# Optimization experiments

Measured on AMD Instinct MI355X. Metric: run time of the kernel, lower is better.

## Reference

```python
import jax, jax.numpy as jnp
import numpy as np

L, BS, D, NH = 1024, 4, 1024, 16
DH = D // NH
H = max(DH, L)  # big=True in DenseSynthesizer -> h = max(head_dim, n_tokens)


def setup_inputs() -> dict:
    key = jax.random.key(0)
    ks = jax.random.split(key, 10)
    s = 0.02
    x = jax.random.normal(ks[0], (L, BS, D), dtype=jnp.float32)
    # additive causal mask (n_tokens, n_tokens)
    causal = jnp.tril(jnp.ones((L, L), dtype=bool))
    attention_mask = jnp.where(causal, 0.0, -1e9).astype(jnp.float32)
    Wi = jax.random.normal(ks[1], (2 * D, D), dtype=jnp.float32) * s
    bi = jnp.zeros((2 * D,), dtype=jnp.float32)
    w1 = jax.random.normal(ks[2], (NH, DH, H), dtype=jnp.float32) * s
    b1 = jnp.zeros((NH, H), dtype=jnp.float32)
    w2 = jax.random.normal(ks[3], (NH, H, L), dtype=jnp.float32) * s
    b2 = jnp.zeros((NH, L), dtype=jnp.float32)
    Wo = jax.random.normal(ks[4], (D, D), dtype=jnp.float32) * s
    bo = jnp.zeros((D,), dtype=jnp.float32)
    return {"x": x, "attention_mask": attention_mask, "Wi": Wi, "bi": bi,
            "w1": w1, "b1": b1, "w2": w2, "b2": b2, "Wo": Wo, "bo": bo}


def reference(x, attention_mask, Wi, bi, w1, b1, w2, b2, Wo, bo):
    l, bs, d = x.shape
    nh, dh, h = w1.shape
    # input projection, chunk into synthesizer input q and values v
    proj = x @ Wi.T + bi                                    # (l, bs, 2d)
    q, v = jnp.split(proj, 2, axis=-1)
    q = q.reshape(l, bs, nh, dh).transpose(1, 0, 2, 3)      # (bs, l, nh, dh)
    v = v.reshape(l, bs * nh, dh).transpose(1, 0, 2)        # (bs*nh, l, dh), n = b*nh + k
    # DenseSynthesizer: per-head two-layer MLP producing attention logits
    hid = jax.nn.relu(jnp.einsum('blkd,kdh->blkh', q, w1) + b1)
    logits = jnp.einsum('blkh,khm->blkm', hid, w2) + b2     # (bs, l, nh, n_tokens)
    logits = logits[..., :l]
    # faithful to torch transpose(0,3).view(l,l,bs*nh).transpose(0,2):
    # flattened batch-head index is m = k*bs + b (head-major)
    logits = logits.transpose(2, 0, 1, 3).reshape(bs * nh, l, l)
    logits = logits + attention_mask[None, :, :]
    probs = jax.nn.softmax(logits, axis=-1)                 # dropout p=0 (eval)
    out = jnp.matmul(probs, v)                              # (bs*nh, l, dh)
    out = out.transpose(1, 0, 2).reshape(l, bs, d)
    return out @ Wo.T + bo
```

## Files before the change

### kernel.cpp

```cpp
#include <hip/hip_runtime.h>

typedef unsigned short u16;
typedef short bf16x8 __attribute__((ext_vector_type(8)));
typedef float f32x4 __attribute__((ext_vector_type(4)));

#define BSZ 4
#define DD 1024
#define LLL 1024

__device__ __forceinline__ float bf2f(u16 u) {
    union { unsigned int i; float f; } w;
    w.i = ((unsigned int)u) << 16;
    return w.f;
}
__device__ __forceinline__ u16 f2bf(float f) {
    union { float fl; unsigned int i; } w;
    w.fl = f;
    w.i += 0x7fffu + ((w.i >> 16) & 1u);
    return (u16)(w.i >> 16);
}

__device__ __forceinline__ void load_lds16(const u16* g, u16* l) {
    __builtin_amdgcn_global_load_lds(
        (const __attribute__((address_space(1))) unsigned int*)g,
        (__attribute__((address_space(3))) unsigned int*)l, 16, 0, 0);
}

__global__ void cvt_all(const float* __restrict__ x, const float* __restrict__ Wi,
                        const float* __restrict__ Wo, u16* __restrict__ xb,
                        u16* __restrict__ wib, u16* __restrict__ wob) {
    int b = blockIdx.x;
    const float* in; u16* out;
    if (b < 4096)      { in = x;  out = xb; }
    else if (b < 6144) { in = Wi; out = wib; b -= 4096; }
    else               { in = Wo; out = wob; b -= 6144; }
    const size_t i = ((size_t)b * 256 + threadIdx.x) * 4;
    const float4 v = *(const float4*)(in + i);
    ushort4 o;
    o.x = f2bf(v.x); o.y = f2bf(v.y); o.z = f2bf(v.z); o.w = f2bf(v.w);
    *(ushort4*)(out + i) = o;
}

__global__ void transpose_cvt(const float* __restrict__ in, u16* __restrict__ out,
                              int R, int C) {
    __shared__ float tile[32][33];
    const size_t base = (size_t)blockIdx.z * R * C;
    const int c0 = blockIdx.x << 5, r0 = blockIdx.y << 5;
    const int tx = threadIdx.x & 31, ty = threadIdx.x >> 5;
    #pragma unroll
    for (int i = 0; i < 32; i += 8)
        tile[ty + i][tx] = in[base + (size_t)(r0 + ty + i) * C + c0 + tx];
    __syncthreads();
    #pragma unroll
    for (int i = 0; i < 32; i += 8)
        out[base + (size_t)(c0 + ty + i) * R + r0 + tx] = f2bf(tile[tx][ty + i]);
}

__global__ void build_vt(const u16* __restrict__ proj, u16* __restrict__ vt) {
    __shared__ u16 tile[64][66];
    const int t = threadIdx.x;
    const int m0 = blockIdx.x << 6;
    const int jj = blockIdx.y;
    const int b = jj >> 4, k = jj & 15;
    const int tx = t & 63, ty = t >> 6;
    #pragma unroll
    for (int mi = ty; mi < 64; mi += 4)
        tile[mi][tx] = proj[(size_t)((m0 + mi) * BSZ + b) * 2048 + 1024 + k * 64 + tx];
    __syncthreads();
    #pragma unroll
    for (int di = ty; di < 64; di += 4)
        vt[((size_t)jj * 80 + di) * 1024 + m0 + tx] = tile[tx][di];
    #pragma unroll
    for (int di = 64 + ty; di < 80; di += 4)
        vt[((size_t)jj * 80 + di) * 1024 + m0 + tx] = (di == 64) ? 0x3F80 : 0;
}

template<int OUT_F32, int RELU>
__global__ __launch_bounds__(256, 2) void gemm_bf16_nt(
    const u16* __restrict__ A, int lda, long long sA,
    const u16* __restrict__ B, int ldb, long long sB,
    const float* __restrict__ bias, int sBias,
    void* __restrict__ C, int ldc, long long sC,
    int K)
{
    __shared__ u16 As[128 * 64];
    __shared__ u16 Bs[128 * 64];
    const int t = threadIdx.x;
    const int z = blockIdx.z;
    const u16* Ab = A + (size_t)z * sA + (size_t)blockIdx.x * 128 * lda;
    const u16* Bb = B + (size_t)z * sB + (size_t)blockIdx.y * 128 * ldb;
    const int wave = t >> 6, lane = t & 63;
    const int wrow = (wave >> 1) << 6;
    const int wcol = (wave & 1) << 6;
    const int lr = lane & 15, lq = lane >> 4;
    const int srow = t >> 3;
    const int gchunk = (t & 7) ^ (srow & 7);
    const u16* ApG = Ab + (size_t)srow * lda + gchunk * 8;
    const u16* BpG = Bb + (size_t)srow * ldb + gchunk * 8;
    u16* AsD = &As[t * 8];
    u16* BsD = &Bs[t * 8];
    const int o0 = ((lq    ) ^ (lr & 7)) * 8;
    const int o1 = ((lq + 4) ^ (lr & 7)) * 8;

    f32x4 acc[4][4];
    #pragma unroll
    for (int i = 0; i < 4; i++)
        #pragma unroll
        for (int j = 0; j < 4; j++)
            acc[i][j] = (f32x4){0.f, 0.f, 0.f, 0.f};

    for (int k0 = 0; k0 < K; k0 += 64) {
        __syncthreads();
        #pragma unroll
        for (int j = 0; j < 4; j++) {
            load_lds16(ApG + (size_t)j * 32 * lda + k0, AsD + j * 2048);
            load_lds16(BpG + (size_t)j * 32 * ldb + k0, BsD + j * 2048);
        }
        __syncthreads();
        #pragma unroll
        for (int s = 0; s < 2; s++) {
            const int oo = s ? o1 : o0;
            bf16x8 af[4], bfv[4];
            #pragma unroll
            for (int i = 0; i < 4; i++)
                af[i] = *(const bf16x8*)&As[(wrow + i * 16 + lr) * 64 + oo];
            #pragma unroll
            for (int j = 0; j < 4; j++)
                bfv[j] = *(const bf16x8*)&Bs[(wcol + j * 16 + lr) * 64 + oo];
            #pragma unroll
            for (int i = 0; i < 4; i++)
                #pragma unroll
                for (int j = 0; j < 4; j++)
                    acc[i][j] = __builtin_amdgcn_mfma_f32_16x16x32_bf16(
                        af[i], bfv[j], acc[i][j], 0, 0, 0);
        }
    }

    const float* biasb = bias + (size_t)z * sBias;
    const size_t row0 = (size_t)blockIdx.x * 128 + wrow + lq * 4;
    const int col0 = blockIdx.y * 128 + wcol + lr;
    #pragma unroll
    for (int j = 0; j < 4; j++) {
        const int col = col0 + j * 16;
        const float bb = biasb[col];
        #pragma unroll
        for (int i = 0; i < 4; i++) {
            #pragma unroll
            for (int r = 0; r < 4; r++) {
                const size_t row = row0 + i * 16 + r;
                float v = acc[i][j][r] + bb;
                if (RELU) v = fmaxf(v, 0.f);
                const size_t idx = row * (size_t)ldc + col;
                if (OUT_F32) ((float*)C)[(size_t)z * sC + idx] = v;
                else         ((u16*)C)[(size_t)z * sC + idx] = f2bf(v);
            }
        }
    }
}

__global__ __launch_bounds__(256, 2) void fused_attn(
    const u16* __restrict__ hid,
    const u16* __restrict__ w2t,
    const float* __restrict__ b2,
    const u16* __restrict__ vt,
    u16* __restrict__ attn)
{
    __shared__ u16 As[64 * 64];
    __shared__ u16 Bs[256 * 64];
    __shared__ u16 Ps[64 * 264];
    const int t = threadIdx.x;
    const int kq = blockIdx.x;
    const int pair = blockIdx.y;
    const int wave = t >> 6, lane = t & 63;
    const int lr = lane & 15, lq = lane >> 4;
    const int wi = wave >> 1, wj = wave & 1;
    const int srow = t >> 3;
    const int gch = (t & 7) ^ (srow & 7);
    const int o0 = ((lq    ) ^ (lr & 7)) * 8;
    const int o1 = ((lq + 4) ^ (lr & 7)) * 8;
    const int bv = kq >> 2;
    const int kvb = 4 * (kq & 3);
    const u16* hb = hid + (size_t)kq * 4194304;
    const u16* wb = w2t + (size_t)kq * 1048576 + (size_t)srow * 1024 + gch * 8;
    const float* b2b = b2 + kq * 1024;

    for (int part = 0; part < 2; part++) {
        const int s = part ? (63 - pair) : pair;
        const int l0 = s << 4;
        const int nt = (s >> 4) + 1;
        const u16* ApG0 = hb + (size_t)((l0 + (srow & 15)) * 4 + (srow >> 4)) * 1024 + gch * 8;
        const u16* ApG1 = ApG0 + (size_t)2 * 1024;
        f32x4 o[5];
        #pragma unroll
        for (int j = 0; j < 5; j++) o[j] = (f32x4){0.f, 0.f, 0.f, 0.f};

        for (int mt = 0; mt < nt; mt++) {
            f32x4 acc[2][8];
            #pragma unroll
            for (int i = 0; i < 2; i++)
                #pragma unroll
                for (int j = 0; j < 8; j++)
                    acc[i][j] = (f32x4){0.f, 0.f, 0.f, 0.f};
            for (int k0 = 0; k0 < 1024; k0 += 64) {
                __syncthreads();
                load_lds16(ApG0 + k0, &As[t * 8]);
                load_lds16(ApG1 + k0, &As[t * 8 + 2048]);
                #pragma unroll
                for (int j2 = 0; j2 < 8; j2++)
                    load_lds16(wb + (size_t)(mt * 256 + j2 * 32) * 1024 + k0,
                               &Bs[j2 * 2048 + t * 8]);
                __syncthreads();
                #pragma unroll
                for (int s2 = 0; s2 < 2; s2++) {
                    const int oo = s2 ? o1 : o0;
                    bf16x8 af[2], bfv[8];
                    #pragma unroll
                    for (int i = 0; i < 2; i++)
                        af[i] = *(const bf16x8*)&As[(wi * 32 + i * 16 + lr) * 64 + oo];
                    #pragma unroll
                    for (int j = 0; j < 8; j++)
                        bfv[j] = *(const bf16x8*)
                            &Bs[(wj * 128 + j * 16 + lr) * 64 + oo];
                    #pragma unroll
                    for (int i = 0; i < 2; i++)
                        #pragma unroll
                        for (int j = 0; j < 8; j++)
                            acc[i][j] = __builtin_amdgcn_mfma_f32_16x16x32_bf16(
                                af[i], bfv[j], acc[i][j], 0, 0, 0);
                }
            }
            __syncthreads();
            float b2v[8];
            #pragma unroll
            for (int j = 0; j < 8; j++)
                b2v[j] = b2b[mt * 256 + wj * 128 + j * 16 + lr];
            #pragma unroll
            for (int i = 0; i < 2; i++) {
                #pragma unroll
                for (int j = 0; j < 8; j++) {
                    const int cp = wj * 128 + j * 16 + lr;
                    const int m = mt * 256 + cp;
                    #pragma unroll
                    for (int rr = 0; rr < 4; rr++) {
                        const int rt = wi * 32 + i * 16 + lq * 4 + rr;
                        const int l = l0 + lq * 4 + rr;
                        const float e = __expf(acc[i][j][rr] + b2v[j]);
                        Ps[rt * 264 + cp] = (m <= l) ? f2bf(e) : (u16)0;
                    }
                }
            }
            __syncthreads();
            {
                const u16* vbb = vt + (size_t)(kq * 4 + wave) * 80 * 1024
                               + (size_t)mt * 256 + lq * 8;
                #pragma unroll
                for (int kc = 0; kc < 8; kc++) {
                    const bf16x8 a = *(const bf16x8*)
                        &Ps[(wave * 16 + lr) * 264 + kc * 32 + lq * 8];
                    #pragma unroll
                    for (int j = 0; j < 5; j++) {
                        const bf16x8 b = *(const bf16x8*)
                            (vbb + (size_t)(j * 16 + lr) * 1024 + kc * 32);
                        o[j] = __builtin_amdgcn_mfma_f32_16x16x32_bf16(
                            a, b, o[j], 0, 0, 0);
                    }
                }
            }
        }
        {
            const int bq = wave;
            float sden[4];
            #pragma unroll
            for (int rr = 0; rr < 4; rr++)
                sden[rr] = __shfl(o[4][rr], lq << 4);
            #pragma unroll
            for (int j = 0; j < 4; j++) {
                #pragma unroll
                for (int rr = 0; rr < 4; rr++) {
                    const int l = l0 + lq * 4 + rr;
                    attn[(size_t)(l * BSZ + bv) * 1024 + (kvb + bq) * 64 + j * 16 + lr]
                        = f2bf(o[j][rr] / sden[rr]);
                }
            }
        }
    }
}

extern "C" void kernel_launch(void* const* d_in, const int* in_sizes, int n_in,
                              void* d_out, int out_size, void* d_ws, size_t ws_size,
                              hipStream_t stream)
{
    (void)in_sizes; (void)n_in; (void)out_size; (void)ws_size;
    const float* x  = (const float*)d_in[0];
    const float* Wi = (const float*)d_in[2];
    const float* bi = (const float*)d_in[3];
    const float* w1 = (const float*)d_in[4];
    const float* b1 = (const float*)d_in[5];
    const float* w2 = (const float*)d_in[6];
    const float* b2 = (const float*)d_in[7];
    const float* Wo = (const float*)d_in[8];
    const float* bo = (const float*)d_in[9];

    u16* x_b    = (u16*)d_ws;
    u16* Wi_b   = x_b    + (size_t)4194304;
    u16* w1t    = Wi_b   + (size_t)2097152;
    u16* w2t    = w1t    + (size_t)1048576;
    u16* Wo_b   = w2t    + (size_t)16777216;
    u16* proj_b = Wo_b   + (size_t)1048576;
    u16* attn_b = proj_b + (size_t)8388608;
    u16* vt     = attn_b + (size_t)4194304;
    u16* hid_a  = vt     + (size_t)5242880;

    cvt_all<<<7168, 256, 0, stream>>>(x, Wi, Wo, x_b, Wi_b, Wo_b);
    transpose_cvt<<<dim3(32,  2, 16), 256, 0, stream>>>(w1, w1t, 64,   1024);
    transpose_cvt<<<dim3(32, 32, 16), 256, 0, stream>>>(w2, w2t, 1024, 1024);

    gemm_bf16_nt<0, 0><<<dim3(32, 16, 1), 256, 0, stream>>>(
        x_b, 1024, 0, Wi_b, 1024, 0, bi, 0, (void*)proj_b, 2048, 0, 1024);

    build_vt<<<dim3(16, 64), 256, 0, stream>>>(proj_b, vt);

    gemm_bf16_nt<0, 1><<<dim3(32, 8, 16), 256, 0, stream>>>(
        proj_b, 2048, 64,
        w1t, 64, 65536,
        b1, 1024,
        (void*)hid_a, 1024, 4194304, 64);

    fused_attn<<<dim3(16, 32), 256, 0, stream>>>(hid_a, w2t, b2, vt, attn_b);

    gemm_bf16_nt<1, 0><<<dim3(32, 8, 1), 256, 0, stream>>>(
        attn_b, 1024, 0, Wo_b, 1024, 0, bo, 0, d_out, 1024, 0, 1024);
}
```

Measured before the change: 401.5 us.

## Alias P tile onto B buffer, one strip per block, raise occupancy

```diff
diff --git a/kernel.cpp b/kernel.cpp
--- a/kernel.cpp
+++ b/kernel.cpp
@@ -158,19 +158,18 @@
     }
 }
 
-__global__ __launch_bounds__(256, 2) void fused_attn(
+__global__ __launch_bounds__(256, 4) void fused_attn(
     const u16* __restrict__ hid,
     const u16* __restrict__ w2t,
     const float* __restrict__ b2,
     const u16* __restrict__ vt,
     u16* __restrict__ attn)
 {
-    __shared__ u16 As[64 * 64];
-    __shared__ u16 Bs[256 * 64];
-    __shared__ u16 Ps[64 * 264];
+    __shared__ u16 As2[64 * 64];
+    __shared__ u16 BsPs[256 * 64];
     const int t = threadIdx.x;
     const int kq = blockIdx.x;
-    const int pair = blockIdx.y;
+    const int s = 63 - (int)blockIdx.y;
     const int wave = t >> 6, lane = t & 63;
     const int lr = lane & 15, lq = lane >> 4;
     const int wi = wave >> 1, wj = wave & 1;
@@ -184,103 +183,106 @@
     const u16* wb = w2t + (size_t)kq * 1048576 + (size_t)srow * 1024 + gch * 8;
     const float* b2b = b2 + kq * 1024;
 
-    for (int part = 0; part < 2; part++) {
-        const int s = part ? (63 - pair) : pair;
-        const int l0 = s << 4;
-        const int nt = (s >> 4) + 1;
-        const u16* ApG0 = hb + (size_t)((l0 + (srow & 15)) * 4 + (srow >> 4)) * 1024 + gch * 8;
-        const u16* ApG1 = ApG0 + (size_t)2 * 1024;
-        f32x4 o[5];
-        #pragma unroll
-        for (int j = 0; j < 5; j++) o[j] = (f32x4){0.f, 0.f, 0.f, 0.f};
-
-        for (int mt = 0; mt < nt; mt++) {
-            f32x4 acc[2][8];
-            #pragma unroll
-            for (int i = 0; i < 2; i++)
+    const int l0 = s << 4;
+    const int nt = (s >> 4) + 1;
+    const u16* ApG0 = hb + (size_t)((l0 + (srow & 15)) * 4 + (srow >> 4)) * 1024 + gch * 8;
+    const u16* ApG1 = ApG0 + (size_t)2 * 1024;
+    f32x4 o[5];
+    #pragma unroll
+    for (int j = 0; j < 5; j++) o[j] = (f32x4){0.f, 0.f, 0.f, 0.f};
+
+    for (int mt = 0; mt < nt; mt++) {
+        f32x4 acc[2][8];
+        #pragma unroll
+        for (int i = 0; i < 2; i++)
+            #pragma unroll
+            for (int j = 0; j < 8; j++)
+                acc[i][j] = (f32x4){0.f, 0.f, 0.f, 0.f};
+        for (int k0 = 0; k0 < 1024; k0 += 64) {
+            __syncthreads();
+            load_lds16(ApG0 + k0, &As2[t * 8]);
+            load_lds16(ApG1 + k0, &As2[t * 8 + 2048]);
+            #pragma unroll
+            for (int j2 = 0; j2 < 8; j2++)
+                load_lds16(wb + (size_t)(mt * 256 + j2 * 32) * 1024 + k0,
+                           &BsPs[j2 * 2048 + t * 8]);
+            __syncthreads();
+            __builtin_amdgcn_s_setprio(1);
+            #pragma unroll
+            for (int s2 = 0; s2 < 2; s2++) {
+                const int oo = s2 ? o1 : o0;
+                bf16x8 af[2], bfv[8];
+                #pragma unroll
+                for (int i = 0; i < 2; i++)
+                    af[i] = *(const bf16x8*)&As2[(wi * 32 + i * 16 + lr) * 64 + oo];
                 #pragma unroll
                 for (int j = 0; j < 8; j++)
-                    acc[i][j] = (f32x4){0.f, 0.f, 0.f, 0.f};
-            for (int k0 = 0; k0 < 1024; k0 += 64) {
-                __syncthreads();
-                load_lds16(ApG0 + k0, &As[t * 8]);
-                load_lds16(ApG1 + k0, &As[t * 8 + 2048]);
-                #pragma unroll
-                for (int j2 = 0; j2 < 8; j2++)
-                    load_lds16(wb + (size_t)(mt * 256 + j2 * 32) * 1024 + k0,
-                               &Bs[j2 * 2048 + t * 8]);
-                __syncthreads();
-                #pragma unroll
-                for (int s2 = 0; s2 < 2; s2++) {
-                    const int oo = s2 ? o1 : o0;
-                    bf16x8 af[2], bfv[8];
-                    #pragma unroll
-                    for (int i = 0; i < 2; i++)
-                        af[i] = *(const bf16x8*)&As[(wi * 32 + i * 16 + lr) * 64 + oo];
+                    bfv[j] = *(const bf16x8*)
+                        &BsPs[(wj * 128 + j * 16 + lr) * 64 + oo];
+                #pragma unroll
+                for (int i = 0; i < 2; i++)
                     #pragma unroll
                     for (int j = 0; j < 8; j++)
-                        bfv[j] = *(const bf16x8*)
-                            &Bs[(wj * 128 + j * 16 + lr) * 64 + oo];
-                    #pragma unroll
-                    for (int i = 0; i < 2; i++)
-                        #pragma unroll
-                        for (int j = 0; j < 8; j++)
-                            acc[i][j] = __builtin_amdgcn_mfma_f32_16x16x32_bf16(
-                                af[i], bfv[j], acc[i][j], 0, 0, 0);
+                        acc[i][j] = __builtin_amdgcn_mfma_f32_16x16x32_bf16(
+                            af[i], bfv[j], acc[i][j], 0, 0, 0);
+            }
+            __builtin_amdgcn_s_setprio(0);
+        }
+        __syncthreads();
+        float b2v[8];
+        #pragma unroll
+        for (int j = 0; j < 8; j++)
+            b2v[j] = b2b[mt * 256 + wj * 128 + j * 16 + lr];
+        #pragma unroll
+        for (int i = 0; i < 2; i++) {
+            #pragma unroll
+            for (int j = 0; j < 8; j++) {
+                const int cp = wj * 128 + j * 16 + lr;
+                const int m = mt * 256 + cp;
+                const int cb = cp & 7;
+                const int cc = cp >> 3;
+                #pragma unroll
+                for (int rr = 0; rr < 4; rr++) {
+                    const int rt = wi * 32 + i * 16 + lq * 4 + rr;
+                    const int l = l0 + lq * 4 + rr;
+                    const float e = __expf(acc[i][j][rr] + b2v[j]);
+                    BsPs[rt * 256 + cb + ((cc ^ (rt & 7)) << 3)]
+                        = (m <= l) ? f2bf(e) : (u16)0;
                 }
             }
-            __syncthreads();
-            float b2v[8];
-            #pragma unroll
-            for (int j = 0; j < 8; j++)
-                b2v[j] = b2b[mt * 256 + wj * 128 + j * 16 + lr];
-            #pragma unroll
-            for (int i = 0; i < 2; i++) {
-                #pragma unroll
-                for (int j = 0; j < 8; j++) {
-                    const int cp = wj * 128 + j * 16 + lr;
-                    const int m = mt * 256 + cp;
-                    #pragma unroll
-                    for (int rr = 0; rr < 4; rr++) {
-                        const int rt = wi * 32 + i * 16 + lq * 4 + rr;
-                        const int l = l0 + lq * 4 + rr;
-                        const float e = __expf(acc[i][j][rr] + b2v[j]);
-                        Ps[rt * 264 + cp] = (m <= l) ? f2bf(e) : (u16)0;
-                    }
+        }
+        __syncthreads();
+        {
+            const u16* vbb = vt + (size_t)(kq * 4 + wave) * 80 * 1024
+                           + (size_t)mt * 256 + lq * 8;
+            const int rt = wave * 16 + lr;
+            #pragma unroll
+            for (int kc = 0; kc < 8; kc++) {
+                const bf16x8 a = *(const bf16x8*)
+                    &BsPs[rt * 256 + ((((kc << 2) + lq) ^ (rt & 7)) << 3)];
+                #pragma unroll
+                for (int j = 0; j < 5; j++) {
+                    const bf16x8 b = *(const bf16x8*)
+                        (vbb + (size_t)(j * 16 + lr) * 1024 + kc * 32);
+                    o[j] = __builtin_amdgcn_mfma_f32_16x16x32_bf16(
+                        a, b, o[j], 0, 0, 0);
                 }
             }
-            __syncthreads();
-            {
-                const u16* vbb = vt + (size_t)(kq * 4 + wave) * 80 * 1024
-                               + (size_t)mt * 256 + lq * 8;
-                #pragma unroll
-                for (int kc = 0; kc < 8; kc++) {
-                    const bf16x8 a = *(const bf16x8*)
-                        &Ps[(wave * 16 + lr) * 264 + kc * 32 + lq * 8];
-                    #pragma unroll
-                    for (int j = 0; j < 5; j++) {
-                        const bf16x8 b = *(const bf16x8*)
-                            (vbb + (size_t)(j * 16 + lr) * 1024 + kc * 32);
-                        o[j] = __builtin_amdgcn_mfma_f32_16x16x32_bf16(
-                            a, b, o[j], 0, 0, 0);
-                    }
-                }
-            }
-        }
-        {
-            const int bq = wave;
-            float sden[4];
-            #pragma unroll
-            for (int rr = 0; rr < 4; rr++)
-                sden[rr] = __shfl(o[4][rr], lq << 4);
-            #pragma unroll
-            for (int j = 0; j < 4; j++) {
-                #pragma unroll
-                for (int rr = 0; rr < 4; rr++) {
-                    const int l = l0 + lq * 4 + rr;
-                    attn[(size_t)(l * BSZ + bv) * 1024 + (kvb + bq) * 64 + j * 16 + lr]
-                        = f2bf(o[j][rr] / sden[rr]);
-                }
+        }
+    }
+    {
+        const int bq = wave;
+        float sden[4];
+        #pragma unroll
+        for (int rr = 0; rr < 4; rr++)
+            sden[rr] = __shfl(o[4][rr], lq << 4);
+        #pragma unroll
+        for (int j = 0; j < 4; j++) {
+            #pragma unroll
+            for (int rr = 0; rr < 4; rr++) {
+                const int l = l0 + lq * 4 + rr;
+                attn[(size_t)(l * BSZ + bv) * 1024 + (kvb + bq) * 64 + j * 16 + lr]
+                    = f2bf(o[j][rr] / sden[rr]);
             }
         }
     }
@@ -326,7 +328,7 @@
         b1, 1024,
         (void*)hid_a, 1024, 4194304, 64);
 
-    fused_attn<<<dim3(16, 32), 256, 0, stream>>>(hid_a, w2t, b2, vt, attn_b);
+    fused_attn<<<dim3(16, 64), 256, 0, stream>>>(hid_a, w2t, b2, vt, attn_b);
 
     gemm_bf16_nt<1, 0><<<dim3(32, 8, 1), 256, 0, stream>>>(
         attn_b, 1024, 0, Wo_b, 1024, 0, bo, 0, d_out, 1024, 0, 1024);
```

Result: slower. 537.1 us (+33.8%).

## Double-buffer the logits GEMM LDS tiles with async prefetch across k-steps

Applied to the files above, without the earlier changes.

```diff
diff --git a/kernel.cpp b/kernel.cpp
--- a/kernel.cpp
+++ b/kernel.cpp
@@ -165,9 +165,9 @@
     const u16* __restrict__ vt,
     u16* __restrict__ attn)
 {
-    __shared__ u16 As[64 * 64];
-    __shared__ u16 Bs[256 * 64];
-    __shared__ u16 Ps[64 * 264];
+    __shared__ u16 As2[2 * 4096];
+    __shared__ u16 Bs[2 * 16384];
+    u16* Ps = &Bs[16384];
     const int t = threadIdx.x;
     const int kq = blockIdx.x;
     const int pair = blockIdx.y;
@@ -182,8 +182,9 @@
     const int kvb = 4 * (kq & 3);
     const u16* hb = hid + (size_t)kq * 4194304;
     const u16* wb = w2t + (size_t)kq * 1048576 + (size_t)srow * 1024 + gch * 8;
-    const float* b2b = b2 + kq * 1024;
-
+    const float* b2b = b2 + kq * 1024 + wj * 128 + lr;
+
+    #pragma unroll 1
     for (int part = 0; part < 2; part++) {
         const int s = part ? (63 - pair) : pair;
         const int l0 = s << 4;
@@ -193,70 +194,104 @@
         f32x4 o[5];
         #pragma unroll
         for (int j = 0; j < 5; j++) o[j] = (f32x4){0.f, 0.f, 0.f, 0.f};
-
+        float b2v[8];
+
+        auto STAGE = [&](int bbuf, int mtt, int k0) {
+            load_lds16(ApG0 + k0, &As2[bbuf * 4096 + t * 8]);
+            load_lds16(ApG1 + k0, &As2[bbuf * 4096 + t * 8 + 2048]);
+            #pragma unroll
+            for (int j2 = 0; j2 < 8; j2++)
+                load_lds16(wb + (size_t)(mtt * 256 + j2 * 32) * 1024 + k0,
+                           &Bs[bbuf * 16384 + j2 * 2048 + t * 8]);
+        };
+
+        #pragma unroll 1
         for (int mt = 0; mt < nt; mt++) {
+            if (mt == 0) {
+                #pragma unroll
+                for (int j = 0; j < 8; j++) b2v[j] = b2b[j * 16];
+                __builtin_amdgcn_sched_barrier(0);
+                STAGE(0, 0, 0);
+                STAGE(1, 0, 64);
+                __builtin_amdgcn_sched_barrier(0);
+            }
             f32x4 acc[2][8];
             #pragma unroll
             for (int i = 0; i < 2; i++)
                 #pragma unroll
                 for (int j = 0; j < 8; j++)
                     acc[i][j] = (f32x4){0.f, 0.f, 0.f, 0.f};
-            for (int k0 = 0; k0 < 1024; k0 += 64) {
-                __syncthreads();
-                load_lds16(ApG0 + k0, &As[t * 8]);
-                load_lds16(ApG1 + k0, &As[t * 8 + 2048]);
-                #pragma unroll
-                for (int j2 = 0; j2 < 8; j2++)
-                    load_lds16(wb + (size_t)(mt * 256 + j2 * 32) * 1024 + k0,
-                               &Bs[j2 * 2048 + t * 8]);
-                __syncthreads();
+
+            #pragma unroll
+            for (int i = 0; i < 16; i++) {
+                if (i < 15) asm volatile("s_waitcnt vmcnt(10)" ::: "memory");
+                else        asm volatile("s_waitcnt vmcnt(0)"  ::: "memory");
+                __builtin_amdgcn_sched_barrier(0);
+                __builtin_amdgcn_s_barrier();
+                __builtin_amdgcn_sched_barrier(0);
+                if (i == 15 && mt + 1 < nt) {
+                    STAGE(0, mt + 1, 0);
+                    __builtin_amdgcn_sched_barrier(0);
+                }
+                const u16* Asb = &As2[(i & 1) * 4096];
+                const u16* Bsb = &Bs[(i & 1) * 16384];
+                __builtin_amdgcn_s_setprio(1);
                 #pragma unroll
                 for (int s2 = 0; s2 < 2; s2++) {
                     const int oo = s2 ? o1 : o0;
                     bf16x8 af[2], bfv[8];
                     #pragma unroll
-                    for (int i = 0; i < 2; i++)
-                        af[i] = *(const bf16x8*)&As[(wi * 32 + i * 16 + lr) * 64 + oo];
+                    for (int i2 = 0; i2 < 2; i2++)
+                        af[i2] = *(const bf16x8*)&Asb[(wi * 32 + i2 * 16 + lr) * 64 + oo];
                     #pragma unroll
                     for (int j = 0; j < 8; j++)
-                        bfv[j] = *(const bf16x8*)
-                            &Bs[(wj * 128 + j * 16 + lr) * 64 + oo];
-                    #pragma unroll
-                    for (int i = 0; i < 2; i++)
+                        bfv[j] = *(const bf16x8*)&Bsb[(wj * 128 + j * 16 + lr) * 64 + oo];
+                    #pragma unroll
+                    for (int i2 = 0; i2 < 2; i2++)
                         #pragma unroll
                         for (int j = 0; j < 8; j++)
-                            acc[i][j] = __builtin_amdgcn_mfma_f32_16x16x32_bf16(
-                                af[i], bfv[j], acc[i][j], 0, 0, 0);
-                }
-            }
-            __syncthreads();
-            float b2v[8];
-            #pragma unroll
-            for (int j = 0; j < 8; j++)
-                b2v[j] = b2b[mt * 256 + wj * 128 + j * 16 + lr];
-            #pragma unroll
-            for (int i = 0; i < 2; i++) {
+                            acc[i2][j] = __builtin_amdgcn_mfma_f32_16x16x32_bf16(
+                                af[i2], bfv[j], acc[i2][j], 0, 0, 0);
+                }
+                __builtin_amdgcn_s_setprio(0);
+                __builtin_amdgcn_sched_barrier(0);
+                __builtin_amdgcn_s_barrier();
+                __builtin_amdgcn_sched_barrier(0);
+                if (i < 14) {
+                    STAGE(i & 1, mt, (i + 2) * 64);
+                    __builtin_amdgcn_sched_barrier(0);
+                }
+            }
+            #pragma unroll
+            for (int i2 = 0; i2 < 2; i2++) {
                 #pragma unroll
                 for (int j = 0; j < 8; j++) {
                     const int cp = wj * 128 + j * 16 + lr;
                     const int m = mt * 256 + cp;
+                    const int cb = cp & 7;
+                    const int cc = cp >> 3;
                     #pragma unroll
                     for (int rr = 0; rr < 4; rr++) {
-                        const int rt = wi * 32 + i * 16 + lq * 4 + rr;
+                        const int rt = wi * 32 + i2 * 16 + lq * 4 + rr;
                         const int l = l0 + lq * 4 + rr;
-                        const float e = __expf(acc[i][j][rr] + b2v[j]);
-                        Ps[rt * 264 + cp] = (m <= l) ? f2bf(e) : (u16)0;
+                        const float e = __expf(acc[i2][j][rr] + b2v[j]);
+                        Ps[rt * 256 + cb + ((cc ^ (rt & 7)) << 3)]
+                            = (m <= l) ? f2bf(e) : (u16)0;
                     }
                 }
             }
-            __syncthreads();
+            asm volatile("s_waitcnt lgkmcnt(0)" ::: "memory");
+            __builtin_amdgcn_sched_barrier(0);
+            __builtin_amdgcn_s_barrier();
+            __builtin_amdgcn_sched_barrier(0);
             {
                 const u16* vbb = vt + (size_t)(kq * 4 + wave) * 80 * 1024
                                + (size_t)mt * 256 + lq * 8;
+                const int rt = wave * 16 + lr;
                 #pragma unroll
                 for (int kc = 0; kc < 8; kc++) {
                     const bf16x8 a = *(const bf16x8*)
-                        &Ps[(wave * 16 + lr) * 264 + kc * 32 + lq * 8];
+                        &Ps[rt * 256 + ((((kc << 2) + lq) ^ (rt & 7)) << 3)];
                     #pragma unroll
                     for (int j = 0; j < 5; j++) {
                         const bf16x8 b = *(const bf16x8*)
@@ -265,6 +300,18 @@
                             a, b, o[j], 0, 0, 0);
                     }
                 }
+            }
+            asm volatile("s_waitcnt lgkmcnt(0)" ::: "memory");
+            __builtin_amdgcn_sched_barrier(0);
+            __builtin_amdgcn_s_barrier();
+            __builtin_amdgcn_sched_barrier(0);
+            if (mt + 1 < nt) {
+                #pragma unroll
+                for (int j = 0; j < 8; j++)
+                    b2v[j] = b2b[(mt + 1) * 256 + j * 16];
+                __builtin_amdgcn_sched_barrier(0);
+                STAGE(1, mt + 1, 64);
+                __builtin_amdgcn_sched_barrier(0);
             }
         }
         {
```

Result: slower. 516.9 us (+28.7%).
